# Kernel tuning notes

Hardware: AMD Instinct MI355X
Metric: run time of the kernel (lower is better)

## Reference

```python
import jax, jax.numpy as jnp
import numpy as np

B, L, D = 2, 2048, 1024
H, HD = 16, 64   # num_heads, head_dim
LD = 256         # mla latent dim


def setup_inputs() -> dict:
    key = jax.random.key(0)
    ks = jax.random.split(key, 6)
    s = lambda fan_in: 1.0 / np.sqrt(fan_in)
    x_bld = jax.random.normal(ks[0], (B, L, D), dtype=jnp.float32)
    Wq = jax.random.normal(ks[1], (D, H, HD), dtype=jnp.float32) * s(D)
    Wkv_down = jax.random.normal(ks[2], (D, LD), dtype=jnp.float32) * s(D)
    Wk_up = jax.random.normal(ks[3], (LD, H, HD), dtype=jnp.float32) * s(LD)
    Wv_up = jax.random.normal(ks[4], (LD, H, HD), dtype=jnp.float32) * s(LD)
    Wout = jax.random.normal(ks[5], (H, HD, D), dtype=jnp.float32) * s(H * HD)
    return {"x_bld": x_bld, "Wq": Wq, "Wkv_down": Wkv_down,
            "Wk_up": Wk_up, "Wv_up": Wv_up, "Wout": Wout}


def reference(x_bld, Wq, Wkv_down, Wk_up, Wv_up, Wout):
    # projections
    q_blhd = jnp.einsum('bld,dhk->blhk', x_bld, Wq)
    latent_bll = jnp.einsum('bld,dc->blc', x_bld, Wkv_down)   # [B,L,LD]
    k_blhd = jnp.einsum('blc,chk->blhk', latent_bll, Wk_up)
    v_blhd = jnp.einsum('blc,chk->blhk', latent_bll, Wv_up)
    # attention scores [B,H,L,L]
    attn = jnp.einsum('bqhd,bkhd->bhqk', q_blhd, k_blhd) / jnp.sqrt(
        jnp.asarray(HD, dtype=x_bld.dtype))
    # causal mask (no window)
    l = x_bld.shape[1]
    mask = (jnp.arange(l)[None, :] <= jnp.arange(l)[:, None])[None, None]
    neg_inf = jnp.finfo(attn.dtype).min
    attn = jax.nn.softmax(jnp.where(mask, attn, neg_inf), axis=-1)
    y_blhd = jnp.einsum('bhqk,bkhd->bqhd', attn, v_blhd)
    return jnp.einsum('bqhd,hdo->bqo', y_blhd, Wout)
```

## Files before the change

kernel.cpp:

```cpp
#include <hip/hip_runtime.h>
#include <hip/hip_bf16.h>

#define BB   2
#define LL   2048
#define DD   1024
#define HH   16
#define HDD  64
#define LDIM 256
#define MTOT (BB * LL)

using short8  = __attribute__((ext_vector_type(8))) short;
using floatx4 = __attribute__((ext_vector_type(4))) float;

static __device__ __forceinline__ unsigned short f2bf(float x) {
  __hip_bfloat16 h = __float2bfloat16(x);
  return *reinterpret_cast<unsigned short*>(&h);
}
static __device__ __forceinline__ unsigned int pk_bf16(float a, float b) {
  return (unsigned int)f2bf(a) | ((unsigned int)f2bf(b) << 16);
}
static __device__ __forceinline__ void load_lds16(const unsigned short* g,
                                                  unsigned short* l) {
  __builtin_amdgcn_global_load_lds(
      (const __attribute__((address_space(1))) unsigned int*)g,
      (__attribute__((address_space(3))) unsigned int*)l, 16, 0, 0);
}
template <int N>
static __device__ __forceinline__ void waitcnt_vm() {
  if constexpr (N == 0) asm volatile("s_waitcnt vmcnt(0)" ::: "memory");
  else if constexpr (N == 2) asm volatile("s_waitcnt vmcnt(2)" ::: "memory");
  else if constexpr (N == 4) asm volatile("s_waitcnt vmcnt(4)" ::: "memory");
  else if constexpr (N == 6) asm volatile("s_waitcnt vmcnt(6)" ::: "memory");
  else if constexpr (N == 8) asm volatile("s_waitcnt vmcnt(8)" ::: "memory");
}
static __device__ __forceinline__ void lds_drain_barrier() {
  asm volatile("s_waitcnt lgkmcnt(0)\n\ts_barrier" ::: "memory");
}

__global__ __launch_bounds__(256) void cast_bf16(const float* __restrict__ in,
                                                 unsigned short* __restrict__ out,
                                                 int n4) {
  const int i = (blockIdx.x * 256 + threadIdx.x);
  if (i < n4) {
    float4 v = ((const float4*)in)[i];
    ushort4 o;
    o.x = f2bf(v.x); o.y = f2bf(v.y); o.z = f2bf(v.z); o.w = f2bf(v.w);
    ((ushort4*)out)[i] = o;
  }
}

__global__ __launch_bounds__(256) void transpose_cast5(
    const float* __restrict__ Wq, const float* __restrict__ Wkv,
    const float* __restrict__ Wku, const float* __restrict__ Wvu,
    const float* __restrict__ Wo,
    unsigned short* __restrict__ WqT, unsigned short* __restrict__ WkvT,
    unsigned short* __restrict__ WkuT, unsigned short* __restrict__ WvuT,
    unsigned short* __restrict__ WoT) {
  const float* src; unsigned short* dst; int R, C;
  switch (blockIdx.z) {
    case 0:  src = Wq;  dst = WqT;  R = 1024; C = 1024; break;
    case 1:  src = Wkv; dst = WkvT; R = 1024; C = 256;  break;
    case 2:  src = Wku; dst = WkuT; R = 256;  C = 1024; break;
    case 3:  src = Wvu; dst = WvuT; R = 256;  C = 1024; break;
    default: src = Wo;  dst = WoT;  R = 1024; C = 1024; break;
  }
  if ((int)blockIdx.x * 32 >= C || (int)blockIdx.y * 32 >= R) return;

  __shared__ float tile[32][33];
  const int tx = threadIdx.x, ty = threadIdx.y;
#pragma unroll
  for (int i = 0; i < 4; ++i) {
    const int r = blockIdx.y * 32 + ty + i * 8;
    tile[ty + i * 8][tx] = src[(size_t)r * C + blockIdx.x * 32 + tx];
  }
  __syncthreads();
#pragma unroll
  for (int i = 0; i < 4; ++i) {
    const int c = blockIdx.x * 32 + ty + i * 8;
    dst[(size_t)c * R + blockIdx.y * 32 + tx] = f2bf(tile[tx][ty + i * 8]);
  }
}

template <int KIND, int BMT, int BNT, int BKT, int NW = 4>
__global__ __launch_bounds__(NW * 64) void gemm2(const unsigned short* __restrict__ A,
                                                 const unsigned short* __restrict__ Bt0,
                                                 const unsigned short* __restrict__ Bt1,
                                                 void* __restrict__ C0,
                                                 void* __restrict__ C1,
                                                 int M, int N, int K, int nsplit) {
  constexpr int WC = NW / 2;
  constexpr int IM = (BMT / 2) / 16;
  constexpr int JN = (BNT / WC) / 16;
  constexpr int TA = BMT * BKT, TB = BNT * BKT;
  constexpr int EPR = NW * 512;
  constexpr int NIA = TA / EPR, NIB = TB / EPR;
  constexpr int NLD = NIA + NIB;
  constexpr int RPI = EPR / BKT;
  __shared__ __align__(16) unsigned short As[2 * TA];
  __shared__ __align__(16) unsigned short Bs[2 * TB];

  const int tid  = threadIdx.x;
  const int w    = tid >> 6;
  const int lane = tid & 63;
  const int lo   = lane & 15;
  const int g    = lane >> 4;
  const int wr   = w / WC, wc = w % WC;
  const int row0  = blockIdx.x * BMT;
  const int col0g = blockIdx.y * BNT;
  const bool second = (col0g >= nsplit);
  const unsigned short* Btp = second ? Bt1 : Bt0;
  const int col0 = second ? col0g - nsplit : col0g;

  floatx4 acc[IM][JN];
#pragma unroll
  for (int i = 0; i < IM; ++i)
#pragma unroll
    for (int j = 0; j < JN; ++j) acc[i][j] = (floatx4){0.f, 0.f, 0.f, 0.f};

  const int sr = (BKT == 32) ? (tid >> 2) : (tid >> 3);
  const int sc = (BKT == 32) ? (tid & 3) : (tid & 7);

  auto swz = [](int chunk, int row) {
    if constexpr (BKT == 32) return chunk ^ ((row >> 1) & 3);
    else                     return chunk ^ (row & 7);
  };

  auto stage = [&](int buf, int k0) {
#pragma unroll
    for (int inst = 0; inst < NIA; ++inst) {
      const int r  = inst * RPI + sr;
      const int cs = swz(sc, r);
      load_lds16(A + (size_t)(row0 + r) * K + k0 + cs * 8,
                 As + buf * TA + inst * EPR + w * 512);
    }
#pragma unroll
    for (int inst = 0; inst < NIB; ++inst) {
      const int r  = inst * RPI + sr;
      const int cs = swz(sc, r);
      load_lds16(Btp + (size_t)(col0 + r) * K + k0 + cs * 8,
                 Bs + buf * TB + inst * EPR + w * 512);
    }
  };

  const int nk = K / BKT;
  stage(0, 0);
  for (int it = 0; it < nk; ++it) {
    const int cur = it & 1;
    if (it + 1 < nk) {
      stage(cur ^ 1, (it + 1) * BKT);
      waitcnt_vm<NLD>();
    } else {
      waitcnt_vm<0>();
    }
    asm volatile("s_barrier" ::: "memory");

    const unsigned short* Ac = As + cur * TA;
    const unsigned short* Bc = Bs + cur * TB;
#pragma unroll
    for (int kk = 0; kk < BKT / 32; ++kk) {
      short8 af[IM], bf[JN];
#pragma unroll
      for (int i = 0; i < IM; ++i) {
        const int rm = (BMT / 2) * wr + 16 * i + lo;
        af[i] = *(const short8*)(Ac + (size_t)rm * BKT + swz(kk * 4 + g, rm) * 8);
      }
#pragma unroll
      for (int j = 0; j < JN; ++j) {
        const int rn = (BNT / WC) * wc + 16 * j + lo;
        bf[j] = *(const short8*)(Bc + (size_t)rn * BKT + swz(kk * 4 + g, rn) * 8);
      }
#pragma unroll
      for (int i = 0; i < IM; ++i)
#pragma unroll
        for (int j = 0; j < JN; ++j)
          acc[i][j] = __builtin_amdgcn_mfma_f32_16x16x32_bf16(af[i], bf[j], acc[i][j], 0, 0, 0);
    }

    lds_drain_barrier();
  }

#pragma unroll
  for (int i = 0; i < IM; ++i) {
    const int mbase = row0 + (BMT / 2) * wr + 16 * i + g * 4;
#pragma unroll
    for (int j = 0; j < JN; ++j) {
      const int nl = col0 + (BNT / WC) * wc + 16 * j + lo;
      const int bq = mbase >> 11, hh = nl >> 6, d = nl & 63;
      if (KIND == 2 && second) {
        const int l = mbase & 2047;
        uint2 o;
        o.x = pk_bf16(acc[i][j][0], acc[i][j][1]);
        o.y = pk_bf16(acc[i][j][2], acc[i][j][3]);
        *(uint2*)(&((unsigned short*)C1)[((size_t)(bq * HH + hh) * HDD + d) * LL + l]) = o;
      } else {
#pragma unroll
        for (int r = 0; r < 4; ++r) {
          const float v = acc[i][j][r];
          const int mm = mbase + r;
          const int l = mm & 2047;
          if (KIND == 0) {
            ((float*)C0)[(size_t)mm * N + nl] = v;
          } else if (KIND == 1) {
            if (!second)
              ((unsigned short*)C0)[((size_t)(bq * HH + hh) * LL + l) * HDD + d] = f2bf(v);
            else
              ((unsigned short*)C1)[(size_t)mm * LDIM + nl] = f2bf(v);
          } else {
            ((unsigned short*)C0)[((size_t)(bq * HH + hh) * LL + l) * HDD + d] = f2bf(v);
          }
        }
      }
    }
  }
}

#define SC2 0.18033688011112042f

__global__ __launch_bounds__(512, 4) void flash_mfma13(const unsigned short* __restrict__ Qh,
                                                       const unsigned short* __restrict__ Kh,
                                                       const unsigned short* __restrict__ Vt,
                                                       unsigned short* __restrict__ y) {
  const int w    = threadIdx.x >> 6;
  const int lane = threadIdx.x & 63;
  const int lo   = lane & 15;
  const int g    = lane >> 4;
  const int kw   = w >> 2;
  const int wq   = w & 3;
  const int h    = blockIdx.x;
  const int b    = blockIdx.y;
  const int pair = blockIdx.z;
  const int qtH  = 31 - pair;
  const int qtL  = pair;

  __shared__ __align__(16) unsigned short Ks[4 * 64 * 64];
  __shared__ __align__(16) unsigned short Vs[4 * 64 * 64];
  __shared__ __align__(16) unsigned short Pq[8][2][16 * 32];

  const size_t bh = (size_t)(b * HH + h);
  const unsigned short* Qp = Qh + bh * LL * HDD;
  const unsigned short* Kp = Kh + bh * LL * HDD;
  const unsigned short* Vp = Vt + bh * (size_t)HDD * LL;
  unsigned short* PwH = Pq[w][0];
  unsigned short* PwL = Pq[w][1];

  const int qHw = qtH * 64 + wq * 16;
  const int qLw = qtL * 64 + wq * 16;

  short8 qfH0 = *(const short8*)(Qp + (size_t)(qHw + lo) * HDD + g * 8);
  short8 qfH1 = *(const short8*)(Qp + (size_t)(qHw + lo) * HDD + 32 + g * 8);
  short8 qfL0 = *(const short8*)(Qp + (size_t)(qLw + lo) * HDD + g * 8);
  short8 qfL1 = *(const short8*)(Qp + (size_t)(qLw + lo) * HDD + 32 + g * 8);

  floatx4 otH[4], otL[4];
#pragma unroll
  for (int ds = 0; ds < 4; ++ds) {
    otH[ds] = (floatx4){0.f, 0.f, 0.f, 0.f};
    otL[ds] = (floatx4){0.f, 0.f, 0.f, 0.f};
  }
  float lsumH = 0.f, lsumL = 0.f;

  const int srow = lane >> 3;
  const int sch  = lane & 7;

  auto stage = [&](int buf, int k0) {
    const int row = w * 8 + srow;
    const int cs  = sch ^ (row & 7);
    load_lds16(Kp + (size_t)(k0 + row) * HDD + cs * 8, Ks + buf * 4096 + w * 512);
    load_lds16(Vp + (size_t)row * LL + k0 + cs * 8,    Vs + buf * 4096 + w * 512);
  };

  auto tile_body = [&](int it, int buf) {
    const unsigned short* Kc = Ks + buf * 4096;
    const unsigned short* Vc = Vs + buf * 4096;
    const int k0  = it * 64;
    const bool doL = (it <= qtL);
    const bool mH  = (it == qtH);
    const bool mL  = (it == qtL);

    floatx4 stH[2], stL[2];
    __builtin_amdgcn_s_setprio(1);
#pragma unroll
    for (int ks = 0; ks < 2; ++ks) {
      const int rm = kw * 32 + ks * 16 + lo;
      short8 a0 = *(const short8*)(Kc + rm * 64 + ((g ^ (rm & 7)) * 8));
      short8 a1 = *(const short8*)(Kc + rm * 64 + (((4 + g) ^ (rm & 7)) * 8));
      floatx4 s = (floatx4){0.f, 0.f, 0.f, 0.f};
      s = __builtin_amdgcn_mfma_f32_16x16x32_bf16(a0, qfH0, s, 0, 0, 0);
      s = __builtin_amdgcn_mfma_f32_16x16x32_bf16(a1, qfH1, s, 0, 0, 0);
      stH[ks] = s;
      if (doL) {
        floatx4 t = (floatx4){0.f, 0.f, 0.f, 0.f};
        t = __builtin_amdgcn_mfma_f32_16x16x32_bf16(a0, qfL0, t, 0, 0, 0);
        t = __builtin_amdgcn_mfma_f32_16x16x32_bf16(a1, qfL1, t, 0, 0, 0);
        stL[ks] = t;
      }
    }
    __builtin_amdgcn_s_setprio(0);

    auto sm = [&](floatx4* st, unsigned short* P, float& lsum, int qw,
                  bool masked) {
      if (!masked) {
#pragma unroll
        for (int ks = 0; ks < 2; ++ks) {
          float p[4];
#pragma unroll
          for (int r = 0; r < 4; ++r) {
            p[r] = __builtin_amdgcn_exp2f(st[ks][r] * SC2);
            lsum += p[r];
          }
          uint2 w2;
          w2.x = pk_bf16(p[0], p[1]);
          w2.y = pk_bf16(p[2], p[3]);
          *(uint2*)(P + lo * 32 + (((ks * 2 + (g >> 1)) ^ (lo & 3)) * 8) + (g & 1) * 4) = w2;
        }
      } else {
        const int qq = qw + lo;
#pragma unroll
        for (int ks = 0; ks < 2; ++ks) {
          float p[4];
#pragma unroll
          for (int r = 0; r < 4; ++r) {
            const int kk = k0 + kw * 32 + ks * 16 + g * 4 + r;
            const float e = __builtin_amdgcn_exp2f(st[ks][r] * SC2);
            p[r] = (kk <= qq) ? e : 0.f;
            lsum += p[r];
          }
          uint2 w2;
          w2.x = pk_bf16(p[0], p[1]);
          w2.y = pk_bf16(p[2], p[3]);
          *(uint2*)(P + lo * 32 + (((ks * 2 + (g >> 1)) ^ (lo & 3)) * 8) + (g & 1) * 4) = w2;
        }
      }
    };
    sm(stH, PwH, lsumH, qHw, mH);
    if (doL) sm(stL, PwL, lsumL, qLw, mL);

    short8 pfH = *(const short8*)(PwH + lo * 32 + ((g ^ (lo & 3)) * 8));
    short8 pfL;
    if (doL) pfL = *(const short8*)(PwL + lo * 32 + ((g ^ (lo & 3)) * 8));
    __builtin_amdgcn_s_setprio(1);
#pragma unroll
    for (int ds = 0; ds < 4; ++ds) {
      const int rm = ds * 16 + lo;
      short8 v = *(const short8*)(Vc + rm * 64 + (((kw * 4 + g) ^ (rm & 7)) * 8));
      otH[ds] = __builtin_amdgcn_mfma_f32_16x16x32_bf16(v, pfH, otH[ds], 0, 0, 0);
      if (doL)
        otL[ds] = __builtin_amdgcn_mfma_f32_16x16x32_bf16(v, pfL, otL[ds], 0, 0, 0);
    }
    __builtin_amdgcn_s_setprio(0);
  };

  const int ntiles = qtH + 1;
  const int np  = ntiles >> 1;
  const bool odd = (ntiles & 1);

  stage(0, 0); stage(1, 64); stage(2, 128); stage(3, 192);

  for (int j = 0; j < np; ++j) {
    const int t0 = 2 * j;
    if (j + 1 < np)      waitcnt_vm<4>();
    else if (odd)        waitcnt_vm<2>();
    else                 waitcnt_vm<0>();
    asm volatile("s_barrier" ::: "memory");

    tile_body(t0,     t0 & 3);
    tile_body(t0 + 1, (t0 + 1) & 3);

    lds_drain_barrier();
    const int tp = t0 + 4;
    if (tp < ntiles)     stage(tp & 3, tp * 64);
    if (tp + 1 < ntiles) stage((tp + 1) & 3, (tp + 1) * 64);
  }
  if (odd) {
    const int t = ntiles - 1;
    waitcnt_vm<0>();
    asm volatile("s_barrier" ::: "memory");
    tile_body(t, t & 3);
    lds_drain_barrier();
  }

  float sH = lsumH; sH += __shfl_xor(sH, 16); sH += __shfl_xor(sH, 32);
  float sL = lsumL; sL += __shfl_xor(sL, 16); sL += __shfl_xor(sL, 32);
  float* oshH = (float*)Ks;
  float* oshL = (float*)Vs;
  float* lsh  = (float*)&Pq[0][0][0];

  if (kw == 1) {
    const int base = (wq * 64 + lane) * 16;
#pragma unroll
    for (int ds = 0; ds < 4; ++ds) {
      *(floatx4*)(oshH + base + ds * 4) = otH[ds];
      *(floatx4*)(oshL + base + ds * 4) = otL[ds];
    }
    if (lane < 16) {
      lsh[wq * 16 + lane]      = sH;
      lsh[64 + wq * 16 + lane] = sL;
    }
  }
  __syncthreads();
  if (kw == 0) {
    const int base = (wq * 64 + lane) * 16;
#pragma unroll
    for (int ds = 0; ds < 4; ++ds) {
      otH[ds] += *(const floatx4*)(oshH + base + ds * 4);
      otL[ds] += *(const floatx4*)(oshL + base + ds * 4);
    }
    sH += lsh[wq * 16 + lo];
    sL += lsh[64 + wq * 16 + lo];

    auto finish = [&](floatx4* ot, float stot, int qw) {
      const float inv = 1.0f / stot;
#pragma unroll
      for (int ds = 0; ds < 4; ++ds) {
        uint2 o;
        o.x = pk_bf16(ot[ds][0] * inv, ot[ds][1] * inv);
        o.y = pk_bf16(ot[ds][2] * inv, ot[ds][3] * inv);
        *(uint2*)(y + (size_t)(b * LL + qw + lo) * (HH * HDD) + h * HDD + ds * 16 + g * 4) = o;
      }
    };
    finish(otH, sH, qHw);
    finish(otL, sL, qLw);
  }
}

extern "C" void kernel_launch(void* const* d_in, const int* in_sizes, int n_in,
                              void* d_out, int out_size, void* d_ws, size_t ws_size,
                              hipStream_t stream) {
  const float* x   = (const float*)d_in[0];
  const float* Wq  = (const float*)d_in[1];
  const float* Wkv = (const float*)d_in[2];
  const float* Wku = (const float*)d_in[3];
  const float* Wvu = (const float*)d_in[4];
  const float* Wo  = (const float*)d_in[5];
  float* out = (float*)d_out;

  unsigned short* xb     = (unsigned short*)d_ws;
  unsigned short* WqT    = xb + (size_t)MTOT * DD;
  unsigned short* WkvT   = WqT + 1024 * 1024;
  unsigned short* WkuT   = WkvT + 256 * 1024;
  unsigned short* WvuT   = WkuT + 1024 * 256;
  unsigned short* WoT    = WvuT + 1024 * 256;
  unsigned short* latent = WoT + 1024 * 1024;
  unsigned short* Qh     = latent + (size_t)MTOT * LDIM;
  unsigned short* Kh     = Qh + (size_t)MTOT * DD;
  unsigned short* Vt     = Kh + (size_t)MTOT * DD;
  unsigned short* y      = Vt + (size_t)MTOT * DD;

  cast_bf16<<<dim3(MTOT * DD / 1024), dim3(256), 0, stream>>>(x, xb, MTOT * DD / 4);
  transpose_cast5<<<dim3(32, 32, 5), dim3(32, 8), 0, stream>>>(
      Wq, Wkv, Wku, Wvu, Wo, WqT, WkvT, WkuT, WvuT, WoT);

  gemm2<1, 128, 64, 64><<<dim3(MTOT / 128, 1280 / 64), dim3(256), 0, stream>>>(
      xb, WqT, WkvT, Qh, latent, MTOT, 1280, DD, 1024);
  gemm2<2, 128, 128, 64><<<dim3(MTOT / 128, 2048 / 128), dim3(256), 0, stream>>>(
      latent, WkuT, WvuT, Kh, Vt, MTOT, 2048, LDIM, 1024);

  flash_mfma13<<<dim3(HH, BB, 16), dim3(512), 0, stream>>>(Qh, Kh, Vt, y);

  gemm2<0, 128, 64, 64><<<dim3(MTOT / 128, DD / 64), dim3(256), 0, stream>>>(
      y, WoT, nullptr, out, nullptr, MTOT, DD, DD, DD);
}
```

Baseline: 160.9 us.

## Fuse prep kernels and swap GEMM operand roles for vectorized epilogue stores

Merges the x cast and the weight transpose-casts into one prep launch with a flattened grid, removing one kernel launch. For the QKV-down and output-projection GEMMs, operands are swapped so that weights supply the M dimension and activations the N dimension, computing the transposed product. Each lane's four accumulator rows then become contiguous in the output, so the epilogue writes packed uint2 bf16 or float4 stores instead of scalar scattered stores. The tile shape and grid mapping change as a result, which may affect L2 reuse of the operands.

```diff
diff --git a/kernel.cpp b/kernel.cpp
--- a/kernel.cpp
+++ b/kernel.cpp
@@ -37,54 +37,54 @@
   asm volatile("s_waitcnt lgkmcnt(0)\n\ts_barrier" ::: "memory");
 }
 
-__global__ __launch_bounds__(256) void cast_bf16(const float* __restrict__ in,
-                                                 unsigned short* __restrict__ out,
-                                                 int n4) {
-  const int i = (blockIdx.x * 256 + threadIdx.x);
-  if (i < n4) {
-    float4 v = ((const float4*)in)[i];
-    ushort4 o;
-    o.x = f2bf(v.x); o.y = f2bf(v.y); o.z = f2bf(v.z); o.w = f2bf(v.w);
-    ((ushort4*)out)[i] = o;
-  }
-}
-
-__global__ __launch_bounds__(256) void transpose_cast5(
-    const float* __restrict__ Wq, const float* __restrict__ Wkv,
-    const float* __restrict__ Wku, const float* __restrict__ Wvu,
-    const float* __restrict__ Wo,
+__global__ __launch_bounds__(256) void prep(
+    const float* __restrict__ x, const float* __restrict__ Wq,
+    const float* __restrict__ Wkv, const float* __restrict__ Wku,
+    const float* __restrict__ Wvu, const float* __restrict__ Wo,
+    unsigned short* __restrict__ xb,
     unsigned short* __restrict__ WqT, unsigned short* __restrict__ WkvT,
     unsigned short* __restrict__ WkuT, unsigned short* __restrict__ WvuT,
     unsigned short* __restrict__ WoT) {
+  const int bid = blockIdx.x;
+  if (bid < 4096) {
+    const int i = bid * 256 + threadIdx.x;
+    float4 v = ((const float4*)x)[i];
+    ushort4 o;
+    o.x = f2bf(v.x); o.y = f2bf(v.y); o.z = f2bf(v.z); o.w = f2bf(v.w);
+    ((ushort4*)xb)[i] = o;
+    return;
+  }
+  const int id = bid - 4096;
+  const int bz = id >> 10, rem = id & 1023, by = rem >> 5, bx = rem & 31;
   const float* src; unsigned short* dst; int R, C;
-  switch (blockIdx.z) {
+  switch (bz) {
     case 0:  src = Wq;  dst = WqT;  R = 1024; C = 1024; break;
     case 1:  src = Wkv; dst = WkvT; R = 1024; C = 256;  break;
     case 2:  src = Wku; dst = WkuT; R = 256;  C = 1024; break;
     case 3:  src = Wvu; dst = WvuT; R = 256;  C = 1024; break;
     default: src = Wo;  dst = WoT;  R = 1024; C = 1024; break;
   }
-  if ((int)blockIdx.x * 32 >= C || (int)blockIdx.y * 32 >= R) return;
+  if (bx * 32 >= C || by * 32 >= R) return;
 
   __shared__ float tile[32][33];
-  const int tx = threadIdx.x, ty = threadIdx.y;
+  const int tx = threadIdx.x & 31, ty = threadIdx.x >> 5;
 #pragma unroll
   for (int i = 0; i < 4; ++i) {
-    const int r = blockIdx.y * 32 + ty + i * 8;
-    tile[ty + i * 8][tx] = src[(size_t)r * C + blockIdx.x * 32 + tx];
+    const int r = by * 32 + ty + i * 8;
+    tile[ty + i * 8][tx] = src[(size_t)r * C + bx * 32 + tx];
   }
   __syncthreads();
 #pragma unroll
   for (int i = 0; i < 4; ++i) {
-    const int c = blockIdx.x * 32 + ty + i * 8;
-    dst[(size_t)c * R + blockIdx.y * 32 + tx] = f2bf(tile[tx][ty + i * 8]);
+    const int c = bx * 32 + ty + i * 8;
+    dst[(size_t)c * R + by * 32 + tx] = f2bf(tile[tx][ty + i * 8]);
   }
 }
 
 template <int KIND, int BMT, int BNT, int BKT, int NW = 4>
-__global__ __launch_bounds__(NW * 64) void gemm2(const unsigned short* __restrict__ A,
-                                                 const unsigned short* __restrict__ Bt0,
-                                                 const unsigned short* __restrict__ Bt1,
+__global__ __launch_bounds__(NW * 64) void gemm2(const unsigned short* __restrict__ P0,
+                                                 const unsigned short* __restrict__ P1,
+                                                 const unsigned short* __restrict__ P2,
                                                  void* __restrict__ C0,
                                                  void* __restrict__ C1,
                                                  int M, int N, int K, int nsplit) {
@@ -107,9 +107,25 @@
   const int wr   = w / WC, wc = w % WC;
   const int row0  = blockIdx.x * BMT;
   const int col0g = blockIdx.y * BNT;
-  const bool second = (col0g >= nsplit);
-  const unsigned short* Btp = second ? Bt1 : Bt0;
-  const int col0 = second ? col0g - nsplit : col0g;
+
+  bool second = false;
+  const unsigned short* Mp;
+  const unsigned short* Np;
+  int arow0 = row0, col0 = col0g;
+  if constexpr (KIND == 2) {
+    second = (col0g >= nsplit);
+    Mp = P0;
+    Np = second ? P2 : P1;
+    col0 = second ? col0g - nsplit : col0g;
+  } else if constexpr (KIND == 1) {
+    second = (row0 >= nsplit);
+    Mp = second ? P2 : P1;
+    if (second) arow0 = row0 - nsplit;
+    Np = P0;
+  } else {
+    Mp = P1;
+    Np = P0;
+  }
 
   floatx4 acc[IM][JN];
 #pragma unroll
@@ -130,14 +146,14 @@
     for (int inst = 0; inst < NIA; ++inst) {
       const int r  = inst * RPI + sr;
       const int cs = swz(sc, r);
-      load_lds16(A + (size_t)(row0 + r) * K + k0 + cs * 8,
+      load_lds16(Mp + (size_t)(arow0 + r) * K + k0 + cs * 8,
                  As + buf * TA + inst * EPR + w * 512);
     }
 #pragma unroll
     for (int inst = 0; inst < NIB; ++inst) {
       const int r  = inst * RPI + sr;
       const int cs = swz(sc, r);
-      load_lds16(Btp + (size_t)(col0 + r) * K + k0 + cs * 8,
+      load_lds16(Np + (size_t)(col0 + r) * K + k0 + cs * 8,
                  Bs + buf * TB + inst * EPR + w * 512);
     }
   };
@@ -181,34 +197,44 @@
 
 #pragma unroll
   for (int i = 0; i < IM; ++i) {
-    const int mbase = row0 + (BMT / 2) * wr + 16 * i + g * 4;
+    const int mg = row0 + (BMT / 2) * wr + 16 * i + g * 4;
 #pragma unroll
     for (int j = 0; j < JN; ++j) {
-      const int nl = col0 + (BNT / WC) * wc + 16 * j + lo;
-      const int bq = mbase >> 11, hh = nl >> 6, d = nl & 63;
-      if (KIND == 2 && second) {
-        const int l = mbase & 2047;
+      if constexpr (KIND == 2) {
+        const int nl = col0 + (BNT / WC) * wc + 16 * j + lo;
+        const int bq = mg >> 11, hh = nl >> 6, d = nl & 63;
+        if (second) {
+          const int l = mg & 2047;
+          uint2 o;
+          o.x = pk_bf16(acc[i][j][0], acc[i][j][1]);
+          o.y = pk_bf16(acc[i][j][2], acc[i][j][3]);
+          *(uint2*)(&((unsigned short*)C1)[((size_t)(bq * HH + hh) * HDD + d) * LL + l]) = o;
+        } else {
+#pragma unroll
+          for (int r = 0; r < 4; ++r) {
+            const int l = (mg + r) & 2047;
+            const int bq2 = (mg + r) >> 11;
+            ((unsigned short*)C0)[((size_t)(bq2 * HH + hh) * LL + l) * HDD + d] =
+                f2bf(acc[i][j][r]);
+          }
+        }
+      } else if constexpr (KIND == 1) {
+        const int ng = col0g + (BNT / WC) * wc + 16 * j + lo;
         uint2 o;
         o.x = pk_bf16(acc[i][j][0], acc[i][j][1]);
         o.y = pk_bf16(acc[i][j][2], acc[i][j][3]);
-        *(uint2*)(&((unsigned short*)C1)[((size_t)(bq * HH + hh) * HDD + d) * LL + l]) = o;
+        if (!second) {
+          const int bq = ng >> 11, ll = ng & 2047, hh = mg >> 6, d = mg & 63;
+          *(uint2*)(&((unsigned short*)C0)[((size_t)(bq * HH + hh) * LL + ll) * HDD + d]) = o;
+        } else {
+          *(uint2*)(&((unsigned short*)C1)[(size_t)ng * LDIM + (mg - nsplit)]) = o;
+        }
       } else {
-#pragma unroll
-        for (int r = 0; r < 4; ++r) {
-          const float v = acc[i][j][r];
-          const int mm = mbase + r;
-          const int l = mm & 2047;
-          if (KIND == 0) {
-            ((float*)C0)[(size_t)mm * N + nl] = v;
-          } else if (KIND == 1) {
-            if (!second)
-              ((unsigned short*)C0)[((size_t)(bq * HH + hh) * LL + l) * HDD + d] = f2bf(v);
-            else
-              ((unsigned short*)C1)[(size_t)mm * LDIM + nl] = f2bf(v);
-          } else {
-            ((unsigned short*)C0)[((size_t)(bq * HH + hh) * LL + l) * HDD + d] = f2bf(v);
-          }
-        }
+        const int ng = col0g + (BNT / WC) * wc + 16 * j + lo;
+        float4 f;
+        f.x = acc[i][j][0]; f.y = acc[i][j][1];
+        f.z = acc[i][j][2]; f.w = acc[i][j][3];
+        *(float4*)(&((float*)C0)[(size_t)ng * M + mg]) = f;
       }
     }
   }
@@ -446,17 +472,16 @@
   unsigned short* Vt     = Kh + (size_t)MTOT * DD;
   unsigned short* y      = Vt + (size_t)MTOT * DD;
 
-  cast_bf16<<<dim3(MTOT * DD / 1024), dim3(256), 0, stream>>>(x, xb, MTOT * DD / 4);
-  transpose_cast5<<<dim3(32, 32, 5), dim3(32, 8), 0, stream>>>(
-      Wq, Wkv, Wku, Wvu, Wo, WqT, WkvT, WkuT, WvuT, WoT);
-
-  gemm2<1, 128, 64, 64><<<dim3(MTOT / 128, 1280 / 64), dim3(256), 0, stream>>>(
-      xb, WqT, WkvT, Qh, latent, MTOT, 1280, DD, 1024);
+  prep<<<dim3(4096 + 5120), dim3(256), 0, stream>>>(
+      x, Wq, Wkv, Wku, Wvu, Wo, xb, WqT, WkvT, WkuT, WvuT, WoT);
+
+  gemm2<1, 128, 64, 64><<<dim3(1280 / 128, MTOT / 64), dim3(256), 0, stream>>>(
+      xb, WqT, WkvT, Qh, latent, 1280, MTOT, DD, 1024);
   gemm2<2, 128, 128, 64><<<dim3(MTOT / 128, 2048 / 128), dim3(256), 0, stream>>>(
       latent, WkuT, WvuT, Kh, Vt, MTOT, 2048, LDIM, 1024);
 
   flash_mfma13<<<dim3(HH, BB, 16), dim3(512), 0, stream>>>(Qh, Kh, Vt, y);
 
-  gemm2<0, 128, 64, 64><<<dim3(MTOT / 128, DD / 64), dim3(256), 0, stream>>>(
-      y, WoT, nullptr, out, nullptr, MTOT, DD, DD, DD);
-}
+  gemm2<0, 128, 64, 64><<<dim3(DD / 128, MTOT / 64), dim3(256), 0, stream>>>(
+      y, WoT, nullptr, out, nullptr, DD, MTOT, DD, 0);
+}
```

Measured after the change: 166.3 us. +3.4%, slower.

## Merge prep kernels and switch flash attention to double-buffered KV staging

Applied to the files above, without the earlier changes.

Merges the x cast and the weight transpose-cast into one launch using a flat block index, which saves one kernel launch. The flash attention kernel drops from a 4-deep K/V LDS ring to a 2-deep double buffer that prefetches one tile ahead, and its launch-bounds occupancy hint rises from 4 to 6. The smaller LDS footprint is meant to allow more resident blocks per CU. In exchange there is less prefetch depth to hide global load latency, and a barrier now runs per tile instead of per pair of tiles.

```diff
diff --git a/kernel.cpp b/kernel.cpp
--- a/kernel.cpp
+++ b/kernel.cpp
@@ -37,47 +37,47 @@
   asm volatile("s_waitcnt lgkmcnt(0)\n\ts_barrier" ::: "memory");
 }
 
-__global__ __launch_bounds__(256) void cast_bf16(const float* __restrict__ in,
-                                                 unsigned short* __restrict__ out,
-                                                 int n4) {
-  const int i = (blockIdx.x * 256 + threadIdx.x);
-  if (i < n4) {
-    float4 v = ((const float4*)in)[i];
-    ushort4 o;
-    o.x = f2bf(v.x); o.y = f2bf(v.y); o.z = f2bf(v.z); o.w = f2bf(v.w);
-    ((ushort4*)out)[i] = o;
-  }
-}
-
-__global__ __launch_bounds__(256) void transpose_cast5(
-    const float* __restrict__ Wq, const float* __restrict__ Wkv,
-    const float* __restrict__ Wku, const float* __restrict__ Wvu,
-    const float* __restrict__ Wo,
+__global__ __launch_bounds__(256) void prep(
+    const float* __restrict__ x, const float* __restrict__ Wq,
+    const float* __restrict__ Wkv, const float* __restrict__ Wku,
+    const float* __restrict__ Wvu, const float* __restrict__ Wo,
+    unsigned short* __restrict__ xb,
     unsigned short* __restrict__ WqT, unsigned short* __restrict__ WkvT,
     unsigned short* __restrict__ WkuT, unsigned short* __restrict__ WvuT,
     unsigned short* __restrict__ WoT) {
+  const int bid = blockIdx.x;
+  if (bid < 4096) {
+    const int i = bid * 256 + threadIdx.x;
+    float4 v = ((const float4*)x)[i];
+    ushort4 o;
+    o.x = f2bf(v.x); o.y = f2bf(v.y); o.z = f2bf(v.z); o.w = f2bf(v.w);
+    ((ushort4*)xb)[i] = o;
+    return;
+  }
+  const int id = bid - 4096;
+  const int bz = id >> 10, rem = id & 1023, by = rem >> 5, bx = rem & 31;
   const float* src; unsigned short* dst; int R, C;
-  switch (blockIdx.z) {
+  switch (bz) {
     case 0:  src = Wq;  dst = WqT;  R = 1024; C = 1024; break;
     case 1:  src = Wkv; dst = WkvT; R = 1024; C = 256;  break;
     case 2:  src = Wku; dst = WkuT; R = 256;  C = 1024; break;
     case 3:  src = Wvu; dst = WvuT; R = 256;  C = 1024; break;
     default: src = Wo;  dst = WoT;  R = 1024; C = 1024; break;
   }
-  if ((int)blockIdx.x * 32 >= C || (int)blockIdx.y * 32 >= R) return;
+  if (bx * 32 >= C || by * 32 >= R) return;
 
   __shared__ float tile[32][33];
-  const int tx = threadIdx.x, ty = threadIdx.y;
+  const int tx = threadIdx.x & 31, ty = threadIdx.x >> 5;
 #pragma unroll
   for (int i = 0; i < 4; ++i) {
-    const int r = blockIdx.y * 32 + ty + i * 8;
-    tile[ty + i * 8][tx] = src[(size_t)r * C + blockIdx.x * 32 + tx];
+    const int r = by * 32 + ty + i * 8;
+    tile[ty + i * 8][tx] = src[(size_t)r * C + bx * 32 + tx];
   }
   __syncthreads();
 #pragma unroll
   for (int i = 0; i < 4; ++i) {
-    const int c = blockIdx.x * 32 + ty + i * 8;
-    dst[(size_t)c * R + blockIdx.y * 32 + tx] = f2bf(tile[tx][ty + i * 8]);
+    const int c = bx * 32 + ty + i * 8;
+    dst[(size_t)c * R + by * 32 + tx] = f2bf(tile[tx][ty + i * 8]);
   }
 }
 
@@ -216,7 +216,7 @@
 
 #define SC2 0.18033688011112042f
 
-__global__ __launch_bounds__(512, 4) void flash_mfma13(const unsigned short* __restrict__ Qh,
+__global__ __launch_bounds__(512, 6) void flash_mfma14(const unsigned short* __restrict__ Qh,
                                                        const unsigned short* __restrict__ Kh,
                                                        const unsigned short* __restrict__ Vt,
                                                        unsigned short* __restrict__ y) {
@@ -232,8 +232,8 @@
   const int qtH  = 31 - pair;
   const int qtL  = pair;
 
-  __shared__ __align__(16) unsigned short Ks[4 * 64 * 64];
-  __shared__ __align__(16) unsigned short Vs[4 * 64 * 64];
+  __shared__ __align__(16) unsigned short Ks[2 * 64 * 64];
+  __shared__ __align__(16) unsigned short Vs[2 * 64 * 64];
   __shared__ __align__(16) unsigned short Pq[8][2][16 * 32];
 
   const size_t bh = (size_t)(b * HH + h);
@@ -351,31 +351,19 @@
   };
 
   const int ntiles = qtH + 1;
-  const int np  = ntiles >> 1;
-  const bool odd = (ntiles & 1);
-
-  stage(0, 0); stage(1, 64); stage(2, 128); stage(3, 192);
-
-  for (int j = 0; j < np; ++j) {
-    const int t0 = 2 * j;
-    if (j + 1 < np)      waitcnt_vm<4>();
-    else if (odd)        waitcnt_vm<2>();
-    else                 waitcnt_vm<0>();
+  stage(0, 0);
+  for (int it = 0; it < ntiles; ++it) {
+    const int cur = it & 1;
+    if (it + 1 < ntiles) {
+      stage(cur ^ 1, (it + 1) * 64);
+      waitcnt_vm<2>();
+    } else {
+      waitcnt_vm<0>();
+    }
     asm volatile("s_barrier" ::: "memory");
 
-    tile_body(t0,     t0 & 3);
-    tile_body(t0 + 1, (t0 + 1) & 3);
-
-    lds_drain_barrier();
-    const int tp = t0 + 4;
-    if (tp < ntiles)     stage(tp & 3, tp * 64);
-    if (tp + 1 < ntiles) stage((tp + 1) & 3, (tp + 1) * 64);
-  }
-  if (odd) {
-    const int t = ntiles - 1;
-    waitcnt_vm<0>();
-    asm volatile("s_barrier" ::: "memory");
-    tile_body(t, t & 3);
+    tile_body(it, cur);
+
     lds_drain_barrier();
   }
 
@@ -446,16 +434,15 @@
   unsigned short* Vt     = Kh + (size_t)MTOT * DD;
   unsigned short* y      = Vt + (size_t)MTOT * DD;
 
-  cast_bf16<<<dim3(MTOT * DD / 1024), dim3(256), 0, stream>>>(x, xb, MTOT * DD / 4);
-  transpose_cast5<<<dim3(32, 32, 5), dim3(32, 8), 0, stream>>>(
-      Wq, Wkv, Wku, Wvu, Wo, WqT, WkvT, WkuT, WvuT, WoT);
+  prep<<<dim3(4096 + 5120), dim3(256), 0, stream>>>(
+      x, Wq, Wkv, Wku, Wvu, Wo, xb, WqT, WkvT, WkuT, WvuT, WoT);
 
   gemm2<1, 128, 64, 64><<<dim3(MTOT / 128, 1280 / 64), dim3(256), 0, stream>>>(
       xb, WqT, WkvT, Qh, latent, MTOT, 1280, DD, 1024);
   gemm2<2, 128, 128, 64><<<dim3(MTOT / 128, 2048 / 128), dim3(256), 0, stream>>>(
       latent, WkuT, WvuT, Kh, Vt, MTOT, 2048, LDIM, 1024);
 
-  flash_mfma13<<<dim3(HH, BB, 16), dim3(512), 0, stream>>>(Qh, Kh, Vt, y);
+  flash_mfma14<<<dim3(HH, BB, 16), dim3(512), 0, stream>>>(Qh, Kh, Vt, y);
 
   gemm2<0, 128, 64, 64><<<dim3(MTOT / 128, DD / 64), dim3(256), 0, stream>>>(
       y, WoT, nullptr, out, nullptr, MTOT, DD, DD, DD);
```

Result: slower. 192.3 us (+19.5%).
